# Kernel tuning notes

Measured on AMD Instinct MI355X. Metric: run time of the kernel, lower is better.

## Reference

```python
import jax, jax.numpy as jnp
import numpy as np

# Model dims (see init_kwargs)
NU = 4096   # num_users (one-hot feature dim)
NV = 4096   # num_items
C = 5       # num_classes (rating levels)
H0 = 256    # hidden[0]
H1 = 128    # hidden[1]
D_IN = 512  # input_dim (side-feature dense dim)
SIDE = 1024 # raw side-feature dim (u_features.size(1))
NB = 2      # nb basis matrices in bilinear decoder


def setup_inputs() -> dict:
    key = jax.random.key(0)
    ks = jax.random.split(key, 16)
    u = jax.random.randint(ks[0], (4096,), 0, NU)
    v = jax.random.randint(ks[1], (4096,), 0, NV)
    r = jax.random.randint(ks[2], (4096,), 0, C)  # unused by forward (as in source)
    raw = jax.random.randint(ks[3], (NU, NV), 0, 4 * C)
    adj_matrix = (raw[None, :, :] == jnp.arange(1, C + 1)[:, None, None]).astype(jnp.float32)
    u_features = jax.random.normal(ks[4], (NU, SIDE), jnp.float32)
    v_features = jax.random.normal(ks[5], (NV, SIDE), jnp.float32)
    def w(k, shape, fan):
        return jax.random.normal(k, shape, jnp.float32) / np.float32(np.sqrt(fan))
    u_w = w(ks[6], (C, NU, H0), NU)          # per-relation GraphConvolution user weights
    v_w = w(ks[7], (C, NV, H0), NV)          # per-relation item weights
    Wu1 = w(ks[8], (D_IN, SIDE), SIDE); bu1 = jnp.zeros((D_IN,), jnp.float32)
    Wv1 = w(ks[9], (D_IN, SIDE), SIDE); bv1 = jnp.zeros((D_IN,), jnp.float32)
    Wu2 = w(ks[10], (H1, D_IN + H0), D_IN + H0)
    Wv2 = w(ks[11], (H1, D_IN + H0), D_IN + H0)
    P = w(ks[12], (NB, H1, H1), H1)          # bilinear basis matrices
    a = w(ks[13], (NB, C), NB)               # basis -> class coefficients
    return dict(u=u, v=v, r=r, adj_matrix=adj_matrix, u_features=u_features,
                v_features=v_features, u_w=u_w, v_w=v_w, Wu1=Wu1, bu1=bu1,
                Wv1=Wv1, bv1=bv1, Wu2=Wu2, Wv2=Wv2, P=P, a=a)


def reference(u, v, r, adj_matrix, u_features, v_features, u_w, v_w,
              Wu1, bu1, Wv1, bv1, Wu2, Wv2, P, a):
    # m = adj[:, u][:, :, v]  -> [C, nu, nv]
    m = adj_matrix[:, u][:, :, v]
    # degree normalization exactly as written in gc_encoder
    du = jnp.abs(m.sum(axis=1).sum(axis=0))   # [nv]
    di = jnp.abs(m.sum(axis=2).sum(axis=0))   # [nu]
    c = 1.0 / jnp.concatenate([du, di], axis=0)
    c = jnp.where(jnp.isinf(c), jnp.zeros_like(c), c)
    # ordinal weight sharing: W_r = sum_{s<=r} Theta_s; one-hot feat @ W == gather rows
    cu = jnp.cumsum(u_w, axis=0)              # [C, NU, H0]
    cv = jnp.cumsum(v_w, axis=0)
    u_x = cu[:, u]                            # [C, nu, H0]
    v_x = cv[:, v]                            # [C, nv, H0]
    # accumulate per-relation message passing across all C relations at once
    u_next = jnp.einsum('ruv,rvh->uh', m, v_x)   # [nu, H0]
    v_next = jnp.einsum('ruv,ruh->vh', m, u_x)   # [nv, H0]
    z = jax.nn.relu(jnp.concatenate([u_next, v_next], axis=0) * c[:, None])
    nu = u.shape[0]
    u_z, v_z = z[:nu], z[nu:]
    u_f = jax.nn.relu(u_features[u] @ Wu1.T + bu1)
    v_f = jax.nn.relu(v_features[v] @ Wv1.T + bv1)
    u_h = jax.nn.relu(jnp.concatenate([u_z, u_f], axis=1) @ Wu2.T)   # [nu, H1]
    v_h = jax.nn.relu(jnp.concatenate([v_z, v_f], axis=1) @ Wv2.T)   # [nv, H1]
    # bilinear mixture decoder: logits[c,u,v] = sum_b a[b,c] * u_h Q_b v_h^T
    outputs = jnp.einsum('ud,bde,ve,bc->cuv', u_h, P, v_h, a)        # [C, nu, nv]
    logp = jax.nn.log_softmax(outputs, axis=0)
    prob = jnp.exp(logp)
    ratings = jnp.arange(1, C + 1, dtype=outputs.dtype)
    m_hat = jnp.einsum('c,cuv->uv', ratings, prob)
    # losses over observed entries
    mask = m.sum(axis=0) > 0
    n_obs = jnp.maximum(mask.sum(), 1).astype(outputs.dtype)
    loss = -(m * logp).sum() / n_obs
    target = (jnp.argmax(m, axis=0) + 1).astype(outputs.dtype)
    se = jnp.where(mask, (m_hat - target) ** 2, jnp.zeros_like(m_hat))
    rmse_loss = jnp.sqrt(se.sum() / n_obs)
    return (m_hat, loss, rmse_loss)
```

## Files before the change

### kernel.cpp

```cpp
#include <hip/hip_runtime.h>
#include <stdint.h>

#define N4   4096
#define H0   256
#define SIDE 1024
#define DIN  512
#define HCAT 768
#define H1   128
#define NC   5
#define NUV  16777216ULL
#define CAP  1536

typedef __attribute__((ext_vector_type(8))) short short8;
typedef __attribute__((ext_vector_type(4))) float floatx4;

__device__ __forceinline__ unsigned short f2bf(float f) {
    unsigned int u;
    __builtin_memcpy(&u, &f, 4);
    unsigned int r = (u + 0x7FFFu + ((u >> 16) & 1u)) >> 16;
    return (unsigned short)r;
}

__device__ __forceinline__ float bf2f(unsigned short b) {
    unsigned int u = (unsigned int)b << 16;
    float f;
    __builtin_memcpy(&f, &u, 4);
    return f;
}

__global__ __launch_bounds__(256) void k_codeF(const float* __restrict__ adj,
                                               uchar4* __restrict__ code4,
                                               const int* __restrict__ u,
                                               const int* __restrict__ v,
                                               int* __restrict__ cu,
                                               int* __restrict__ cv) {
    int b = blockIdx.x, t = threadIdx.x;
    if (b < 16384) {
        size_t g = (size_t)b * 256 + t;
        size_t base = g * 4;
        uchar4 out = {0, 0, 0, 0};
        #pragma unroll
        for (int c = 0; c < NC; c++) {
            float4 s = *(const float4*)(adj + (size_t)c * NUV + base);
            out.x = (s.x != 0.f) ? (unsigned char)(c + 1) : out.x;
            out.y = (s.y != 0.f) ? (unsigned char)(c + 1) : out.y;
            out.z = (s.z != 0.f) ? (unsigned char)(c + 1) : out.z;
            out.w = (s.w != 0.f) ? (unsigned char)(c + 1) : out.w;
        }
        code4[g] = out;
    } else {
        int i = (b - 16384) * 256 + t;
        atomicAdd(&cu[u[i]], 1);
        atomicAdd(&cv[v[i]], 1);
    }
}

__global__ __launch_bounds__(256) void k_fuse0(const uint8_t* __restrict__ code,
                                               uint8_t* __restrict__ codeT,
                                               const float* __restrict__ u_w,
                                               const int* __restrict__ cnt_u,
                                               unsigned short* __restrict__ T_Au,
                                               const float* __restrict__ v_w,
                                               const int* __restrict__ cnt_v,
                                               unsigned short* __restrict__ T_Bv) {
    __shared__ __align__(16) uint8_t tile[64][80];
    int b = blockIdx.x, t = threadIdx.x;
    if (b < 4096) {
        int bx = b & 63, by = b >> 6;
        int row = t >> 2;
        int seg = (t & 3) * 16;
        int p0 = by * 64, q0 = bx * 64;
        uint4 vdat = *(const uint4*)(code + (size_t)(p0 + row) * N4 + q0 + seg);
        *(uint4*)(&tile[row][seg]) = vdat;
        __syncthreads();
        union { uint4 u4; uint8_t bb[16]; } o;
        #pragma unroll
        for (int l = 0; l < 16; l++) o.bb[l] = tile[seg + l][row];
        *(uint4*)(codeT + (size_t)(q0 + row) * N4 + p0 + seg) = o.u4;
    } else {
        int node = (b - 4096) & 4095;
        int side = (b - 4096) >> 12;
        const float* w = side ? v_w : u_w;
        const int* cnt = side ? cnt_v : cnt_u;
        unsigned short* out = side ? T_Bv : T_Au;
        int h = t;
        float c = (float)cnt[node];
        float acc = 0.f;
        #pragma unroll
        for (int r = 0; r < NC; r++) {
            size_t idx = ((size_t)r * N4 + node) * H0 + h;
            acc += w[idx];
            union { _Float16 h16; unsigned short s; } cvt;
            cvt.h16 = (_Float16)(acc * c);
            out[idx] = cvt.s;
        }
    }
}

__global__ __launch_bounds__(256) void k_prep(const uint8_t* __restrict__ code,
                                              const uint8_t* __restrict__ codeT,
                                              const int* __restrict__ cnt_u,
                                              const int* __restrict__ cnt_v,
                                              unsigned short* __restrict__ idxU,
                                              int* __restrict__ nnzU,
                                              float* __restrict__ rowDeg,
                                              unsigned short* __restrict__ idxV,
                                              int* __restrict__ nnzV,
                                              float* __restrict__ colDeg,
                                              const float* __restrict__ u_feat,
                                              unsigned short* __restrict__ fuhi,
                                              unsigned short* __restrict__ fulo,
                                              const float* __restrict__ v_feat,
                                              unsigned short* __restrict__ fvhi,
                                              unsigned short* __restrict__ fvlo,
                                              const float* __restrict__ Wu1,
                                              unsigned short* __restrict__ wuhi,
                                              unsigned short* __restrict__ wulo,
                                              const float* __restrict__ Wv1,
                                              unsigned short* __restrict__ wvhi,
                                              unsigned short* __restrict__ wvlo,
                                              const float* __restrict__ Wu2,
                                              unsigned short* __restrict__ w2uhi,
                                              unsigned short* __restrict__ w2ulo,
                                              const float* __restrict__ Wv2,
                                              unsigned short* __restrict__ w2vhi,
                                              unsigned short* __restrict__ w2vlo,
                                              const float* __restrict__ P,
                                              unsigned short* __restrict__ pthi,
                                              unsigned short* __restrict__ ptlo) {
    __shared__ float cw[4096];
    __shared__ int wtot[4];
    __shared__ float wdeg[4];
    __shared__ __align__(16) unsigned short ebuf[CAP];
    int b = blockIdx.x, t = threadIdx.x;
    if (b < 8192) {
        int side = b >> 12;
        int p = b & 4095;
        const uint8_t* codeRows = side ? codeT : code;
        const int* cntOther = side ? cnt_u : cnt_v;
        unsigned short* idx = side ? idxV : idxU;
        int* nnz = side ? nnzV : nnzU;
        float* deg = side ? colDeg : rowDeg;

        int lane = t & 63, wv = t >> 6;
        const int4* co4 = (const int4*)cntOther;
        #pragma unroll
        for (int l = 0; l < 4; l++) {
            int4 ci = co4[t + l * 256];
            ((float4*)cw)[t + l * 256] =
                make_float4((float)ci.x, (float)ci.y, (float)ci.z, (float)ci.w);
        }
        uint4 w = ((const uint4*)(codeRows + (size_t)p * N4))[t];
        unsigned char bb[16];
        __builtin_memcpy(bb, &w, 16);
        int cnt = 0;
        #pragma unroll
        for (int j = 0; j < 16; j++) cnt += (bb[j] != 0);
        int sc = cnt;
        #pragma unroll
        for (int off = 1; off < 64; off <<= 1) {
            int up = __shfl_up(sc, off, 64);
            if (lane >= off) sc += up;
        }
        if (lane == 63) wtot[wv] = sc;
        __syncthreads();
        int wbase = 0;
        #pragma unroll
        for (int ww = 0; ww < 4; ww++) wbase += (ww < wv) ? wtot[ww] : 0;
        int total = wtot[0] + wtot[1] + wtot[2] + wtot[3];
        int pos = wbase + sc - cnt;
        float dsum = 0.f;
        #pragma unroll
        for (int j = 0; j < 16; j++) {
            int r = bb[j];
            if (r) {
                int q = t * 16 + j;
                if (pos < CAP) ebuf[pos] = (unsigned short)((r - 1) * N4 + q);
                pos++;
                dsum += cw[q];
            }
        }
        #pragma unroll
        for (int off = 32; off; off >>= 1) dsum += __shfl_down(dsum, off, 64);
        if (lane == 0) wdeg[wv] = dsum;
        __syncthreads();
        int tw = total < CAP ? total : CAP;
        if (t == 0) { deg[p] = wdeg[0] + wdeg[1] + wdeg[2] + wdeg[3]; nnz[p] = tw; }
        for (int e = t; e < tw; e += 256) idx[(size_t)p * CAP + e] = ebuf[e];
        return;
    }
    if (b >= 17600) {
        int tid = (b - 17600) * 256 + t;
        int bb = tid >> 14;
        int d = (tid >> 7) & 127;
        int e = tid & 127;
        float val = P[tid];
        unsigned short hb = f2bf(val);
        size_t o = ((size_t)bb * 128 + e) * 128 + d;
        pthi[o] = hb;
        ptlo[o] = f2bf(val - bf2f(hb));
        return;
    }
    const float* src;
    unsigned short* hi;
    unsigned short* lo;
    int lb;
    if (b < 12288)      { src = u_feat; hi = fuhi; lo = fulo; lb = b - 8192; }
    else if (b < 16384) { src = v_feat; hi = fvhi; lo = fvlo; lb = b - 12288; }
    else if (b < 16896) { src = Wu1; hi = wuhi; lo = wulo; lb = b - 16384; }
    else if (b < 17408) { src = Wv1; hi = wvhi; lo = wvlo; lb = b - 16896; }
    else if (b < 17504) { src = Wu2; hi = w2uhi; lo = w2ulo; lb = b - 17408; }
    else                { src = Wv2; hi = w2vhi; lo = w2vlo; lb = b - 17504; }
    size_t g = ((size_t)lb * 256 + t) * 4;
    float4 x = *(const float4*)(src + g);
    float f[4] = {x.x, x.y, x.z, x.w};
    unsigned short hh[4], ll[4];
    #pragma unroll
    for (int k = 0; k < 4; k++) {
        unsigned short hb = f2bf(f[k]);
        hh[k] = hb;
        ll[k] = f2bf(f[k] - bf2f(hb));
    }
    *(ushort4*)(hi + g) = make_ushort4(hh[0], hh[1], hh[2], hh[3]);
    *(ushort4*)(lo + g) = make_ushort4(ll[0], ll[1], ll[2], ll[3]);
}

__global__ __launch_bounds__(256) void k_gatherE(const unsigned short* __restrict__ idxU,
                                                 const int* __restrict__ nnzU,
                                                 const unsigned short* __restrict__ T_Bv,
                                                 const unsigned short* __restrict__ idxV,
                                                 const int* __restrict__ nnzV,
                                                 const unsigned short* __restrict__ T_Au,
                                                 float* __restrict__ pnn) {
    __shared__ __align__(16) unsigned short sidx[CAP];
    __shared__ float red[16][132];
    __shared__ int sbnd[2];
    int bid = blockIdx.x;
    int side  = bid >> 15;
    int r1    = bid & 32767;
    int epoch = r1 >> 13;
    int r2    = r1 & 8191;
    int p     = r2 >> 1;
    int half  = r2 & 1;

    const unsigned short* idx = side ? idxV : idxU;
    const int* nnz = side ? nnzV : nnzU;
    const char* tb = (const char*)(side ? T_Au : T_Bv);

    int t = threadIdx.x;
    int n = nnz[p];
    const unsigned short* rowIdx = idx + (size_t)p * CAP;
    int nv = (n + 7) >> 3;
    for (int i = t; i < nv; i += 256)
        ((uint4*)sidx)[i] = ((const uint4*)rowIdx)[i];
    __syncthreads();
    if (t < 2) {
        int target = (epoch + t) << 10;
        int lo = 0, hi = n;
        while (lo < hi) {
            int mid = (lo + hi) >> 1;
            int q = sidx[mid] & 4095;
            if (q < target) lo = mid + 1; else hi = mid;
        }
        sbnd[t] = lo;
    }
    __syncthreads();
    int elo = sbnd[0], ehi = sbnd[1];

    int s = t >> 4;
    int c = t & 15;
    int boff = half * 256 + c * 16;
    float acc[8] = {0.f, 0.f, 0.f, 0.f, 0.f, 0.f, 0.f, 0.f};
    int cnt = ehi - elo;
    int nmain = elo + (cnt & ~63);
    for (int e = elo + s; e < nmain; e += 64) {
        int o0 = ((int)sidx[e])      << 9;
        int o1 = ((int)sidx[e + 16]) << 9;
        int o2 = ((int)sidx[e + 32]) << 9;
        int o3 = ((int)sidx[e + 48]) << 9;
        uint4 d0 = *(const uint4*)(tb + o0 + boff);
        uint4 d1 = *(const uint4*)(tb + o1 + boff);
        uint4 d2 = *(const uint4*)(tb + o2 + boff);
        uint4 d3 = *(const uint4*)(tb + o3 + boff);
        union { uint4 u; _Float16 h[8]; } cv;
        cv.u = d0;
        #pragma unroll
        for (int k = 0; k < 8; k++) acc[k] += (float)cv.h[k];
        cv.u = d1;
        #pragma unroll
        for (int k = 0; k < 8; k++) acc[k] += (float)cv.h[k];
        cv.u = d2;
        #pragma unroll
        for (int k = 0; k < 8; k++) acc[k] += (float)cv.h[k];
        cv.u = d3;
        #pragma unroll
        for (int k = 0; k < 8; k++) acc[k] += (float)cv.h[k];
    }
    for (int e = nmain + s; e < ehi; e += 16) {
        int o = ((int)sidx[e]) << 9;
        uint4 d = *(const uint4*)(tb + o + boff);
        union { uint4 u; _Float16 h[8]; } cv;
        cv.u = d;
        #pragma unroll
        for (int k = 0; k < 8; k++) acc[k] += (float)cv.h[k];
    }
    #pragma unroll
    for (int k = 0; k < 8; k++) red[s][c * 8 + k] = acc[k];
    __syncthreads();
    if (t < 128) {
        float sum = 0.f;
        #pragma unroll
        for (int ss = 0; ss < 16; ss++) sum += red[ss][t];
        pnn[(((size_t)(side * 4 + epoch)) * N4 + p) * H0 + half * 128 + t] = sum;
    }
}

__global__ __launch_bounds__(256) void k_l1Z(const unsigned short* __restrict__ fuhi,
                                             const unsigned short* __restrict__ fulo,
                                             const unsigned short* __restrict__ fvhi,
                                             const unsigned short* __restrict__ fvlo,
                                             const int* __restrict__ u,
                                             const int* __restrict__ v,
                                             const unsigned short* __restrict__ wuhi,
                                             const unsigned short* __restrict__ wulo,
                                             const unsigned short* __restrict__ wvhi,
                                             const unsigned short* __restrict__ wvlo,
                                             const float* __restrict__ bu1,
                                             const float* __restrict__ bv1,
                                             unsigned short* __restrict__ chiU,
                                             unsigned short* __restrict__ cloU,
                                             unsigned short* __restrict__ chiV,
                                             unsigned short* __restrict__ cloV,
                                             const float* __restrict__ pnn,
                                             const float* __restrict__ colDeg,
                                             const float* __restrict__ rowDeg,
                                             const uint8_t* __restrict__ code,
                                             uint8_t* __restrict__ codeR) {
    __shared__ __align__(16) unsigned short Bh[64][72];
    __shared__ __align__(16) unsigned short Bl[64][72];
    int b = blockIdx.x, t = threadIdx.x;
    if (b < 1024) {
        int side = b >> 9;
        int rem = b & 511;
        const unsigned short* Ahi = side ? fvhi : fuhi;
        const unsigned short* Alo = side ? fvlo : fulo;
        const int* rowmap = side ? v : u;
        const unsigned short* Bhi = side ? wvhi : wuhi;
        const unsigned short* Blo = side ? wvlo : wulo;
        const float* bias = side ? bv1 : bu1;
        unsigned short* CHi = (side ? chiV : chiU) + H0;
        unsigned short* CLo = (side ? cloV : cloU) + H0;

        int wave = t >> 6, lane = t & 63;
        int lr = lane & 15;
        int lk = lane >> 4;
        int i0 = (rem >> 3) * 64 + wave * 16;
        int n0 = (rem & 7) * 64;
        int gi = rowmap[i0 + lr];
        const unsigned short* pah = Ahi + (size_t)gi * SIDE;
        const unsigned short* pal = Alo + (size_t)gi * SIDE;
        int srow = t >> 2, sseg = (t & 3) * 16;
        floatx4 acc[4];
        #pragma unroll
        for (int jt = 0; jt < 4; jt++) acc[jt] = (floatx4){0.f, 0.f, 0.f, 0.f};
        for (int ks = 0; ks < SIDE / 64; ks++) {
            const unsigned short* sh = Bhi + (size_t)(n0 + srow) * SIDE + ks * 64 + sseg;
            const unsigned short* sl = Blo + (size_t)(n0 + srow) * SIDE + ks * 64 + sseg;
            __syncthreads();
            *(uint4*)(&Bh[srow][sseg]) = *(const uint4*)sh;
            *(uint4*)(&Bh[srow][sseg + 8]) = *(const uint4*)(sh + 8);
            *(uint4*)(&Bl[srow][sseg]) = *(const uint4*)sl;
            *(uint4*)(&Bl[srow][sseg + 8]) = *(const uint4*)(sl + 8);
            __syncthreads();
            #pragma unroll
            for (int kk = 0; kk < 2; kk++) {
                int ko = ks * 64 + kk * 32 + lk * 8;
                short8 ah = *(const short8*)(pah + ko);
                short8 al = *(const short8*)(pal + ko);
                #pragma unroll
                for (int jt = 0; jt < 4; jt++) {
                    short8 bh = *(const short8*)(&Bh[jt * 16 + lr][kk * 32 + lk * 8]);
                    short8 bl = *(const short8*)(&Bl[jt * 16 + lr][kk * 32 + lk * 8]);
                    acc[jt] = __builtin_amdgcn_mfma_f32_16x16x32_bf16(ah, bh, acc[jt], 0, 0, 0);
                    acc[jt] = __builtin_amdgcn_mfma_f32_16x16x32_bf16(ah, bl, acc[jt], 0, 0, 0);
                    acc[jt] = __builtin_amdgcn_mfma_f32_16x16x32_bf16(al, bh, acc[jt], 0, 0, 0);
                }
            }
        }
        #pragma unroll
        for (int jt = 0; jt < 4; jt++) {
            int cn = n0 + jt * 16 + lr;
            float bb = bias[cn];
            #pragma unroll
            for (int r = 0; r < 4; r++) {
                int ci = i0 + lk * 4 + r;
                float vv = fmaxf(acc[jt][r] + bb, 0.f);
                unsigned short hb = f2bf(vv);
                CHi[(size_t)ci * HCAT + cn] = hb;
                CLo[(size_t)ci * HCAT + cn] = f2bf(vv - bf2f(hb));
            }
        }
        return;
    }
    if (b < 9216) {
        int idx = b - 1024;
        int side = idx >> 12;
        int i = idx & 4095;
        const int* idxs = side ? v : u;
        const int* idxo = side ? u : v;
        const float* deg = side ? rowDeg : colDeg;
        unsigned short* catHi = side ? chiV : chiU;
        unsigned short* catLo = side ? cloV : cloU;
        int h = t;
        float d = deg[idxo[i]];
        float inv = d > 0.f ? 1.f / d : 0.f;
        int row = idxs[i];
        const float* pr = pnn + ((size_t)side * 4 * N4 + row) * H0 + h;
        float nnv = 0.f;
        #pragma unroll
        for (int e = 0; e < 4; e++) nnv += pr[(size_t)e * N4 * H0];
        float val = fmaxf(nnv * inv, 0.f);
        unsigned short hb = f2bf(val);
        catHi[(size_t)i * HCAT + h] = hb;
        catLo[(size_t)i * HCAT + h] = f2bf(val - bf2f(hb));
        return;
    }
    uint8_t* rowbuf = (uint8_t*)Bh;
    int i = b - 9216;
    int urow = u[i];
    ((uint4*)rowbuf)[t] = ((const uint4*)(code + (size_t)urow * N4))[t];
    __syncthreads();
    uint8_t ob[16];
    #pragma unroll
    for (int w = 0; w < 4; w++) {
        int4 vv = ((const int4*)v)[t * 4 + w];
        ob[w * 4 + 0] = rowbuf[vv.x];
        ob[w * 4 + 1] = rowbuf[vv.y];
        ob[w * 4 + 2] = rowbuf[vv.z];
        ob[w * 4 + 3] = rowbuf[vv.w];
    }
    uint4 o;
    __builtin_memcpy(&o, ob, 16);
    ((uint4*)(codeR + (size_t)i * N4))[t] = o;
}

__global__ __launch_bounds__(256) void k_l2F(const unsigned short* __restrict__ chiU,
                                             const unsigned short* __restrict__ cloU,
                                             const unsigned short* __restrict__ w2uhi,
                                             const unsigned short* __restrict__ w2ulo,
                                             unsigned short* __restrict__ uhhi,
                                             unsigned short* __restrict__ uhlo,
                                             const unsigned short* __restrict__ chiV,
                                             const unsigned short* __restrict__ cloV,
                                             const unsigned short* __restrict__ w2vhi,
                                             const unsigned short* __restrict__ w2vlo,
                                             unsigned short* __restrict__ vhb) {
    __shared__ __align__(16) unsigned short Bh[64][72];
    __shared__ __align__(16) unsigned short Bl[64][72];
    int side = blockIdx.z;
    const unsigned short* Ahi = side ? chiV : chiU;
    const unsigned short* Alo = side ? cloV : cloU;
    const unsigned short* Bhi = side ? w2vhi : w2uhi;
    const unsigned short* Blo = side ? w2vlo : w2ulo;

    int t = threadIdx.x;
    int wave = t >> 6, lane = t & 63;
    int lr = lane & 15;
    int lk = lane >> 4;
    int i0 = blockIdx.y * 64 + wave * 16;
    int n0 = blockIdx.x * 64;
    const unsigned short* pah = Ahi + (size_t)(i0 + lr) * HCAT;
    const unsigned short* pal = Alo + (size_t)(i0 + lr) * HCAT;
    int srow = t >> 2, sseg = (t & 3) * 16;
    floatx4 acc[4];
    #pragma unroll
    for (int jt = 0; jt < 4; jt++) acc[jt] = (floatx4){0.f, 0.f, 0.f, 0.f};
    for (int ks = 0; ks < HCAT / 64; ks++) {
        const unsigned short* sh = Bhi + (size_t)(n0 + srow) * HCAT + ks * 64 + sseg;
        const unsigned short* sl = Blo + (size_t)(n0 + srow) * HCAT + ks * 64 + sseg;
        __syncthreads();
        *(uint4*)(&Bh[srow][sseg]) = *(const uint4*)sh;
        *(uint4*)(&Bh[srow][sseg + 8]) = *(const uint4*)(sh + 8);
        *(uint4*)(&Bl[srow][sseg]) = *(const uint4*)sl;
        *(uint4*)(&Bl[srow][sseg + 8]) = *(const uint4*)(sl + 8);
        __syncthreads();
        #pragma unroll
        for (int kk = 0; kk < 2; kk++) {
            int ko = ks * 64 + kk * 32 + lk * 8;
            short8 ah = *(const short8*)(pah + ko);
            short8 al = *(const short8*)(pal + ko);
            #pragma unroll
            for (int jt = 0; jt < 4; jt++) {
                short8 bh = *(const short8*)(&Bh[jt * 16 + lr][kk * 32 + lk * 8]);
                short8 bl = *(const short8*)(&Bl[jt * 16 + lr][kk * 32 + lk * 8]);
                acc[jt] = __builtin_amdgcn_mfma_f32_16x16x32_bf16(ah, bh, acc[jt], 0, 0, 0);
                acc[jt] = __builtin_amdgcn_mfma_f32_16x16x32_bf16(ah, bl, acc[jt], 0, 0, 0);
                acc[jt] = __builtin_amdgcn_mfma_f32_16x16x32_bf16(al, bh, acc[jt], 0, 0, 0);
            }
        }
    }
    #pragma unroll
    for (int jt = 0; jt < 4; jt++) {
        int cn = n0 + jt * 16 + lr;
        #pragma unroll
        for (int r = 0; r < 4; r++) {
            int ci = i0 + lk * 4 + r;
            float vv = fmaxf(acc[jt][r], 0.f);
            if (side) {
                vhb[(size_t)ci * H1 + cn] = f2bf(vv);
            } else {
                unsigned short hb = f2bf(vv);
                uhhi[(size_t)ci * H1 + cn] = hb;
                uhlo[(size_t)ci * H1 + cn] = f2bf(vv - bf2f(hb));
            }
        }
    }
}

__global__ __launch_bounds__(256) void k_tb(const unsigned short* __restrict__ uhhi,
                                            const unsigned short* __restrict__ uhlo,
                                            const unsigned short* __restrict__ pthi,
                                            const unsigned short* __restrict__ ptlo,
                                            unsigned short* __restrict__ tbout) {
    __shared__ __align__(16) unsigned short Bh[64][72];
    __shared__ __align__(16) unsigned short Bl[64][72];
    int bmat = blockIdx.z;
    int t = threadIdx.x;
    int wave = t >> 6, lane = t & 63;
    int lr = lane & 15;
    int lk = lane >> 4;
    int i0 = blockIdx.y * 64 + wave * 16;
    int n0 = blockIdx.x * 64;
    const unsigned short* Bhi = pthi + (size_t)bmat * H1 * H1;
    const unsigned short* Blo = ptlo + (size_t)bmat * H1 * H1;
    const unsigned short* pah = uhhi + (size_t)(i0 + lr) * H1;
    const unsigned short* pal = uhlo + (size_t)(i0 + lr) * H1;
    int srow = t >> 2, sseg = (t & 3) * 16;
    floatx4 acc[4];
    #pragma unroll
    for (int jt = 0; jt < 4; jt++) acc[jt] = (floatx4){0.f, 0.f, 0.f, 0.f};
    for (int ks = 0; ks < H1 / 64; ks++) {
        const unsigned short* sh = Bhi + (size_t)(n0 + srow) * H1 + ks * 64 + sseg;
        const unsigned short* sl = Blo + (size_t)(n0 + srow) * H1 + ks * 64 + sseg;
        __syncthreads();
        *(uint4*)(&Bh[srow][sseg]) = *(const uint4*)sh;
        *(uint4*)(&Bh[srow][sseg + 8]) = *(const uint4*)(sh + 8);
        *(uint4*)(&Bl[srow][sseg]) = *(const uint4*)sl;
        *(uint4*)(&Bl[srow][sseg + 8]) = *(const uint4*)(sl + 8);
        __syncthreads();
        #pragma unroll
        for (int kk = 0; kk < 2; kk++) {
            int ko = ks * 64 + kk * 32 + lk * 8;
            short8 ah = *(const short8*)(pah + ko);
            short8 al = *(const short8*)(pal + ko);
            #pragma unroll
            for (int jt = 0; jt < 4; jt++) {
                short8 bh = *(const short8*)(&Bh[jt * 16 + lr][kk * 32 + lk * 8]);
                short8 bl = *(const short8*)(&Bl[jt * 16 + lr][kk * 32 + lk * 8]);
                acc[jt] = __builtin_amdgcn_mfma_f32_16x16x32_bf16(ah, bh, acc[jt], 0, 0, 0);
                acc[jt] = __builtin_amdgcn_mfma_f32_16x16x32_bf16(ah, bl, acc[jt], 0, 0, 0);
                acc[jt] = __builtin_amdgcn_mfma_f32_16x16x32_bf16(al, bh, acc[jt], 0, 0, 0);
            }
        }
    }
    #pragma unroll
    for (int jt = 0; jt < 4; jt++) {
        int cn = n0 + jt * 16 + lr;
        #pragma unroll
        for (int r = 0; r < 4; r++) {
            int ci = i0 + lk * 4 + r;
            tbout[(size_t)bmat * N4 * H1 + (size_t)ci * H1 + cn] = f2bf(acc[jt][r]);
        }
    }
}

__global__ __launch_bounds__(256) void k_scores3(const unsigned short* __restrict__ tb,
                                                 const unsigned short* __restrict__ vhb,
                                                 const uint8_t* __restrict__ codeR,
                                                 const float* __restrict__ a_f,
                                                 float* __restrict__ mhat,
                                                 float* __restrict__ part) {
    __shared__ float wred[4][3];
    int t = threadIdx.x;
    int wave = t >> 6, lane = t & 63;
    int lr = lane & 15;
    int lk = lane >> 4;
    int i0 = blockIdx.y * 64 + wave * 16;
    int j0 = blockIdx.x * 128;
    float sa0[NC], sa1[NC];
    #pragma unroll
    for (int c = 0; c < NC; c++) { sa0[c] = a_f[c]; sa1[c] = a_f[5 + c]; }

    const unsigned short* t0p = tb;
    const unsigned short* t1p = tb + (size_t)N4 * H1;
    short8 a0[4], a1[4];
    #pragma unroll
    for (int kc = 0; kc < 4; kc++) {
        size_t off = (size_t)(i0 + lr) * H1 + kc * 32 + lk * 8;
        a0[kc] = *(const short8*)(t0p + off);
        a1[kc] = *(const short8*)(t1p + off);
    }

    const uint8_t* crbase = codeR + (size_t)(i0 + lk * 4) * N4 + lr;
    short8 bcur[4];
    int cbv[4];
    {
        int jb = j0;
        const uint8_t* crp = crbase + jb;
        cbv[0] = crp[0];
        cbv[1] = crp[N4];
        cbv[2] = crp[2 * N4];
        cbv[3] = crp[3 * N4];
        #pragma unroll
        for (int kc = 0; kc < 4; kc++)
            bcur[kc] = *(const short8*)(vhb + (size_t)(jb + lr) * H1 + kc * 32 + lk * 8);
    }

    float lsum = 0.f, ssum = 0.f, nobs = 0.f;
    for (int jt = 0; jt < 8; jt++) {
        int jb = j0 + jt * 16;
        int j = jb + lr;
        short8 bnext[4];
        int cbn[4];
        if (jt < 7) {
            int jb2 = jb + 16;
            const uint8_t* crp = crbase + jb2;
            cbn[0] = crp[0];
            cbn[1] = crp[N4];
            cbn[2] = crp[2 * N4];
            cbn[3] = crp[3 * N4];
            #pragma unroll
            for (int kc = 0; kc < 4; kc++)
                bnext[kc] = *(const short8*)(vhb + (size_t)(jb2 + lr) * H1 + kc * 32 + lk * 8);
        }
        floatx4 C0 = {0.f, 0.f, 0.f, 0.f}, C1 = {0.f, 0.f, 0.f, 0.f};
        #pragma unroll
        for (int kc = 0; kc < 4; kc++) {
            C0 = __builtin_amdgcn_mfma_f32_16x16x32_bf16(a0[kc], bcur[kc], C0, 0, 0, 0);
            C1 = __builtin_amdgcn_mfma_f32_16x16x32_bf16(a1[kc], bcur[kc], C1, 0, 0, 0);
        }
        #pragma unroll
        for (int r = 0; r < 4; r++) {
            int i = i0 + lk * 4 + r;
            float v0 = C0[r], v1 = C1[r];
            float l[NC];
            float mx = -1e30f;
            #pragma unroll
            for (int c = 0; c < NC; c++) {
                l[c] = sa0[c] * v0 + sa1[c] * v1;
                mx = fmaxf(mx, l[c]);
            }
            float den = 0.f, num = 0.f;
            #pragma unroll
            for (int c = 0; c < NC; c++) {
                float e = __expf(l[c] - mx);
                den += e;
                num += (float)(c + 1) * e;
            }
            float mh = num / den;
            mhat[(size_t)i * N4 + j] = mh;
            int cb = cbv[r];
            if (cb) {
                float lse = mx + __logf(den);
                lsum += lse - l[cb - 1];
                float df = mh - (float)cb;
                ssum += df * df;
                nobs += 1.f;
            }
        }
        if (jt < 7) {
            #pragma unroll
            for (int kc = 0; kc < 4; kc++) bcur[kc] = bnext[kc];
            #pragma unroll
            for (int r = 0; r < 4; r++) cbv[r] = cbn[r];
        }
    }
    #pragma unroll
    for (int off = 32; off; off >>= 1) {
        lsum += __shfl_down(lsum, off, 64);
        ssum += __shfl_down(ssum, off, 64);
        nobs += __shfl_down(nobs, off, 64);
    }
    if (lane == 0) { wred[wave][0] = lsum; wred[wave][1] = ssum; wred[wave][2] = nobs; }
    __syncthreads();
    if (t == 0) {
        int bid = blockIdx.y * gridDim.x + blockIdx.x;
        part[bid * 3 + 0] = wred[0][0] + wred[1][0] + wred[2][0] + wred[3][0];
        part[bid * 3 + 1] = wred[0][1] + wred[1][1] + wred[2][1] + wred[3][1];
        part[bid * 3 + 2] = wred[0][2] + wred[1][2] + wred[2][2] + wred[3][2];
    }
}

__global__ __launch_bounds__(256) void k_finalize(const float* __restrict__ part,
                                                  float* __restrict__ out) {
    __shared__ float sred[3][4];
    int t = threadIdx.x, lane = t & 63, wv = t >> 6;
    float l = 0.f, s = 0.f, n = 0.f;
    for (int i = t; i < 2048; i += 256) {
        l += part[i * 3 + 0];
        s += part[i * 3 + 1];
        n += part[i * 3 + 2];
    }
    #pragma unroll
    for (int off = 32; off; off >>= 1) {
        l += __shfl_down(l, off, 64);
        s += __shfl_down(s, off, 64);
        n += __shfl_down(n, off, 64);
    }
    if (lane == 0) { sred[0][wv] = l; sred[1][wv] = s; sred[2][wv] = n; }
    __syncthreads();
    if (t == 0) {
        float L = sred[0][0] + sred[0][1] + sred[0][2] + sred[0][3];
        float S = sred[1][0] + sred[1][1] + sred[1][2] + sred[1][3];
        float N = fmaxf(sred[2][0] + sred[2][1] + sred[2][2] + sred[2][3], 1.f);
        out[NUV + 0] = L / N;
        out[NUV + 1] = sqrtf(S / N);
    }
}

extern "C" void kernel_launch(void* const* d_in, const int* in_sizes, int n_in,
                              void* d_out, int out_size, void* d_ws, size_t ws_size,
                              hipStream_t stream) {
    const int* u = (const int*)d_in[0];
    const int* v = (const int*)d_in[1];
    const float* adj    = (const float*)d_in[3];
    const float* u_feat = (const float*)d_in[4];
    const float* v_feat = (const float*)d_in[5];
    const float* u_w    = (const float*)d_in[6];
    const float* v_w    = (const float*)d_in[7];
    const float* Wu1    = (const float*)d_in[8];
    const float* bu1    = (const float*)d_in[9];
    const float* Wv1    = (const float*)d_in[10];
    const float* bv1    = (const float*)d_in[11];
    const float* Wu2    = (const float*)d_in[12];
    const float* Wv2    = (const float*)d_in[13];
    const float* P      = (const float*)d_in[14];
    const float* a      = (const float*)d_in[15];
    float* out = (float*)d_out;

    char* ws = (char*)d_ws;
    const size_t O_CODE  = 0;
    const size_t O_CNTU  = 16777216;
    const size_t O_CNTV  = O_CNTU + 16384;
    const size_t O_ACC   = O_CNTV + 16384;
    const size_t O_TAU   = O_ACC + 256;
    const size_t O_TBV   = O_TAU + 10485760;
    const size_t O_IDXU  = O_TBV + 10485760;
    const size_t O_IDXV  = O_IDXU + 12582912;
    const size_t O_NNZU  = O_IDXV + 12582912;
    const size_t O_NNZV  = O_NNZU + 16384;
    const size_t O_RDEG  = O_NNZV + 16384;
    const size_t O_CDEG  = O_RDEG + 16384;
    const size_t O_UNN   = O_CDEG + 16384;
    const size_t O_VNN   = O_UNN + 4194304;
    const size_t O_UCAT  = O_VNN + 4194304;
    const size_t O_VCAT  = O_UCAT + 12582912;
    const size_t O_UH    = O_VCAT + 12582912;
    const size_t O_VHB   = O_UH + 2097152;
    const size_t O_PT    = O_VHB + 1048576;
    const size_t O_TB    = O_PT + 131072;
    const size_t O_CODET = O_UCAT;
    const size_t O_CODER = O_TAU;
    const size_t O_PART  = O_CNTU;
    const size_t O_FULO  = O_UNN;
    const size_t O_CHIU  = O_UCAT;
    const size_t O_CLOU  = O_UCAT + 6291456;
    const size_t O_CHIV  = O_VCAT;
    const size_t O_CLOV  = O_VCAT + 6291456;
    const size_t S_FVHI  = 0;
    const size_t S_FVLO  = 8388608;
    const size_t S_WUHI  = 16777216;
    const size_t S_WULO  = S_WUHI + 1048576;
    const size_t S_WVHI  = S_WULO + 1048576;
    const size_t S_WVLO  = S_WVHI + 1048576;
    const size_t S_W2UHI = S_WVLO + 1048576;
    const size_t S_W2ULO = S_W2UHI + 196608;
    const size_t S_W2VHI = S_W2ULO + 196608;
    const size_t S_W2VLO = S_W2VHI + 196608;
    const size_t S_PNN   = 25165824;
    const size_t S_FUHI  = 58720256;

    uint8_t* code  = (uint8_t*)(ws + O_CODE);
    uint8_t* codeT = (uint8_t*)(ws + O_CODET);
    uint8_t* codeR = (uint8_t*)(ws + O_CODER);
    int* cnt_u = (int*)(ws + O_CNTU);
    int* cnt_v = (int*)(ws + O_CNTV);
    unsigned short* T_Au = (unsigned short*)(ws + O_TAU);
    unsigned short* T_Bv = (unsigned short*)(ws + O_TBV);
    unsigned short* idxU = (unsigned short*)(ws + O_IDXU);
    unsigned short* idxV = (unsigned short*)(ws + O_IDXV);
    int* nnzU = (int*)(ws + O_NNZU);
    int* nnzV = (int*)(ws + O_NNZV);
    float* rowDeg = (float*)(ws + O_RDEG);
    float* colDeg = (float*)(ws + O_CDEG);
    unsigned short* uhhi = (unsigned short*)(ws + O_UH);
    unsigned short* uhlo = (unsigned short*)(ws + O_UH + 1048576);
    unsigned short* vhb = (unsigned short*)(ws + O_VHB);
    unsigned short* pthi = (unsigned short*)(ws + O_PT);
    unsigned short* ptlo = (unsigned short*)(ws + O_PT + 65536);
    unsigned short* tb = (unsigned short*)(ws + O_TB);
    float* part = (float*)(ws + O_PART);
    unsigned short* fulo = (unsigned short*)(ws + O_FULO);
    unsigned short* chiU = (unsigned short*)(ws + O_CHIU);
    unsigned short* cloU = (unsigned short*)(ws + O_CLOU);
    unsigned short* chiV = (unsigned short*)(ws + O_CHIV);
    unsigned short* cloV = (unsigned short*)(ws + O_CLOV);
    char* outc = (char*)d_out;
    unsigned short* fuhi = (unsigned short*)(outc + S_FUHI);
    unsigned short* fvhi = (unsigned short*)(outc + S_FVHI);
    unsigned short* fvlo = (unsigned short*)(outc + S_FVLO);
    unsigned short* wuhi = (unsigned short*)(outc + S_WUHI);
    unsigned short* wulo = (unsigned short*)(outc + S_WULO);
    unsigned short* wvhi = (unsigned short*)(outc + S_WVHI);
    unsigned short* wvlo = (unsigned short*)(outc + S_WVLO);
    unsigned short* w2uhi = (unsigned short*)(outc + S_W2UHI);
    unsigned short* w2ulo = (unsigned short*)(outc + S_W2ULO);
    unsigned short* w2vhi = (unsigned short*)(outc + S_W2VHI);
    unsigned short* w2vlo = (unsigned short*)(outc + S_W2VLO);
    float* pnn = (float*)(outc + S_PNN);

    hipMemsetAsync(ws + O_CNTU, 0, 16384 + 16384, stream);

    k_codeF<<<16400, 256, 0, stream>>>(adj, (uchar4*)code, u, v, cnt_u, cnt_v);
    k_fuse0<<<12288, 256, 0, stream>>>(code, codeT, u_w, cnt_u, T_Au, v_w, cnt_v, T_Bv);
    k_prep<<<17728, 256, 0, stream>>>(code, codeT, cnt_u, cnt_v,
                                      idxU, nnzU, rowDeg, idxV, nnzV, colDeg,
                                      u_feat, fuhi, fulo,
                                      v_feat, fvhi, fvlo,
                                      Wu1, wuhi, wulo, Wv1, wvhi, wvlo,
                                      Wu2, w2uhi, w2ulo, Wv2, w2vhi, w2vlo,
                                      P, pthi, ptlo);
    k_gatherE<<<65536, 256, 0, stream>>>(idxU, nnzU, T_Bv, idxV, nnzV, T_Au, pnn);
    k_l1Z<<<13312, 256, 0, stream>>>(fuhi, fulo, fvhi, fvlo, u, v,
                                     wuhi, wulo, wvhi, wvlo, bu1, bv1,
                                     chiU, cloU, chiV, cloV,
                                     pnn, colDeg, rowDeg, code, codeR);
    k_l2F<<<dim3(2, 64, 2), 256, 0, stream>>>(chiU, cloU, w2uhi, w2ulo, uhhi, uhlo,
                                              chiV, cloV, w2vhi, w2vlo, vhb);
    k_tb<<<dim3(2, 64, 2), 256, 0, stream>>>(uhhi, uhlo, pthi, ptlo, tb);
    k_scores3<<<dim3(32, 64), 256, 0, stream>>>(tb, vhb, codeR, a, out, part);
    k_finalize<<<1, 256, 0, stream>>>(part, out);
}
```

Before: 874.0 us.

## Merge layer-1 GEMM into gather kernel and fold finalize into scores via last-block atomic

The dense layer-1 side-feature GEMM blocks, which do not depend on the gather results, now share a launch with the sparse gather blocks so both run in one grid. The z-normalisation and codeR rows move into a separate k_zR kernel. The single-block finalize kernel is removed: the last k_scores3 block, found with an atomic counter, does the final reduction. This cuts launch gaps and lets the independent GEMM overlap with the gather, but the shared-memory union and atomic counter add a little complexity.

```diff
diff --git a/kernel.cpp b/kernel.cpp
--- a/kernel.cpp
+++ b/kernel.cpp
@@ -225,121 +225,35 @@
     *(ushort4*)(lo + g) = make_ushort4(ll[0], ll[1], ll[2], ll[3]);
 }
 
-__global__ __launch_bounds__(256) void k_gatherE(const unsigned short* __restrict__ idxU,
-                                                 const int* __restrict__ nnzU,
-                                                 const unsigned short* __restrict__ T_Bv,
-                                                 const unsigned short* __restrict__ idxV,
-                                                 const int* __restrict__ nnzV,
-                                                 const unsigned short* __restrict__ T_Au,
-                                                 float* __restrict__ pnn) {
-    __shared__ __align__(16) unsigned short sidx[CAP];
-    __shared__ float red[16][132];
-    __shared__ int sbnd[2];
-    int bid = blockIdx.x;
-    int side  = bid >> 15;
-    int r1    = bid & 32767;
-    int epoch = r1 >> 13;
-    int r2    = r1 & 8191;
-    int p     = r2 >> 1;
-    int half  = r2 & 1;
-
-    const unsigned short* idx = side ? idxV : idxU;
-    const int* nnz = side ? nnzV : nnzU;
-    const char* tb = (const char*)(side ? T_Au : T_Bv);
-
-    int t = threadIdx.x;
-    int n = nnz[p];
-    const unsigned short* rowIdx = idx + (size_t)p * CAP;
-    int nv = (n + 7) >> 3;
-    for (int i = t; i < nv; i += 256)
-        ((uint4*)sidx)[i] = ((const uint4*)rowIdx)[i];
-    __syncthreads();
-    if (t < 2) {
-        int target = (epoch + t) << 10;
-        int lo = 0, hi = n;
-        while (lo < hi) {
-            int mid = (lo + hi) >> 1;
-            int q = sidx[mid] & 4095;
-            if (q < target) lo = mid + 1; else hi = mid;
-        }
-        sbnd[t] = lo;
-    }
-    __syncthreads();
-    int elo = sbnd[0], ehi = sbnd[1];
-
-    int s = t >> 4;
-    int c = t & 15;
-    int boff = half * 256 + c * 16;
-    float acc[8] = {0.f, 0.f, 0.f, 0.f, 0.f, 0.f, 0.f, 0.f};
-    int cnt = ehi - elo;
-    int nmain = elo + (cnt & ~63);
-    for (int e = elo + s; e < nmain; e += 64) {
-        int o0 = ((int)sidx[e])      << 9;
-        int o1 = ((int)sidx[e + 16]) << 9;
-        int o2 = ((int)sidx[e + 32]) << 9;
-        int o3 = ((int)sidx[e + 48]) << 9;
-        uint4 d0 = *(const uint4*)(tb + o0 + boff);
-        uint4 d1 = *(const uint4*)(tb + o1 + boff);
-        uint4 d2 = *(const uint4*)(tb + o2 + boff);
-        uint4 d3 = *(const uint4*)(tb + o3 + boff);
-        union { uint4 u; _Float16 h[8]; } cv;
-        cv.u = d0;
-        #pragma unroll
-        for (int k = 0; k < 8; k++) acc[k] += (float)cv.h[k];
-        cv.u = d1;
-        #pragma unroll
-        for (int k = 0; k < 8; k++) acc[k] += (float)cv.h[k];
-        cv.u = d2;
-        #pragma unroll
-        for (int k = 0; k < 8; k++) acc[k] += (float)cv.h[k];
-        cv.u = d3;
-        #pragma unroll
-        for (int k = 0; k < 8; k++) acc[k] += (float)cv.h[k];
-    }
-    for (int e = nmain + s; e < ehi; e += 16) {
-        int o = ((int)sidx[e]) << 9;
-        uint4 d = *(const uint4*)(tb + o + boff);
-        union { uint4 u; _Float16 h[8]; } cv;
-        cv.u = d;
-        #pragma unroll
-        for (int k = 0; k < 8; k++) acc[k] += (float)cv.h[k];
-    }
-    #pragma unroll
-    for (int k = 0; k < 8; k++) red[s][c * 8 + k] = acc[k];
-    __syncthreads();
-    if (t < 128) {
-        float sum = 0.f;
-        #pragma unroll
-        for (int ss = 0; ss < 16; ss++) sum += red[ss][t];
-        pnn[(((size_t)(side * 4 + epoch)) * N4 + p) * H0 + half * 128 + t] = sum;
-    }
-}
-
-__global__ __launch_bounds__(256) void k_l1Z(const unsigned short* __restrict__ fuhi,
-                                             const unsigned short* __restrict__ fulo,
-                                             const unsigned short* __restrict__ fvhi,
-                                             const unsigned short* __restrict__ fvlo,
-                                             const int* __restrict__ u,
-                                             const int* __restrict__ v,
-                                             const unsigned short* __restrict__ wuhi,
-                                             const unsigned short* __restrict__ wulo,
-                                             const unsigned short* __restrict__ wvhi,
-                                             const unsigned short* __restrict__ wvlo,
-                                             const float* __restrict__ bu1,
-                                             const float* __restrict__ bv1,
-                                             unsigned short* __restrict__ chiU,
-                                             unsigned short* __restrict__ cloU,
-                                             unsigned short* __restrict__ chiV,
-                                             unsigned short* __restrict__ cloV,
-                                             const float* __restrict__ pnn,
-                                             const float* __restrict__ colDeg,
-                                             const float* __restrict__ rowDeg,
-                                             const uint8_t* __restrict__ code,
-                                             uint8_t* __restrict__ codeR) {
-    __shared__ __align__(16) unsigned short Bh[64][72];
-    __shared__ __align__(16) unsigned short Bl[64][72];
+__global__ __launch_bounds__(256) void k_gatherL1(const unsigned short* __restrict__ idxU,
+                                                  const int* __restrict__ nnzU,
+                                                  const unsigned short* __restrict__ T_Bv,
+                                                  const unsigned short* __restrict__ idxV,
+                                                  const int* __restrict__ nnzV,
+                                                  const unsigned short* __restrict__ T_Au,
+                                                  float* __restrict__ pnn,
+                                                  const unsigned short* __restrict__ fuhi,
+                                                  const unsigned short* __restrict__ fulo,
+                                                  const unsigned short* __restrict__ fvhi,
+                                                  const unsigned short* __restrict__ fvlo,
+                                                  const int* __restrict__ u,
+                                                  const int* __restrict__ v,
+                                                  const unsigned short* __restrict__ wuhi,
+                                                  const unsigned short* __restrict__ wulo,
+                                                  const unsigned short* __restrict__ wvhi,
+                                                  const unsigned short* __restrict__ wvlo,
+                                                  const float* __restrict__ bu1,
+                                                  const float* __restrict__ bv1,
+                                                  unsigned short* __restrict__ chiU,
+                                                  unsigned short* __restrict__ cloU,
+                                                  unsigned short* __restrict__ chiV,
+                                                  unsigned short* __restrict__ cloV) {
+    __shared__ __align__(16) char smem[18432];
     int b = blockIdx.x, t = threadIdx.x;
     if (b < 1024) {
+        typedef unsigned short Row72[72];
+        Row72* Bh = (Row72*)smem;
+        Row72* Bl = (Row72*)(smem + 9216);
         int side = b >> 9;
         int rem = b & 511;
         const unsigned short* Ahi = side ? fvhi : fuhi;
@@ -402,10 +316,104 @@
         }
         return;
     }
-    if (b < 9216) {
-        int idx = b - 1024;
-        int side = idx >> 12;
-        int i = idx & 4095;
+    unsigned short* sidx = (unsigned short*)smem;
+    float (*red)[132] = (float(*)[132])(smem + 3072);
+    int* sbnd = (int*)(smem + 3072 + 8448);
+    int bid = b - 1024;
+    int side  = bid >> 15;
+    int r1    = bid & 32767;
+    int epoch = r1 >> 13;
+    int r2    = r1 & 8191;
+    int p     = r2 >> 1;
+    int half  = r2 & 1;
+
+    const unsigned short* idx = side ? idxV : idxU;
+    const int* nnz = side ? nnzV : nnzU;
+    const char* tb = (const char*)(side ? T_Au : T_Bv);
+
+    int n = nnz[p];
+    const unsigned short* rowIdx = idx + (size_t)p * CAP;
+    int nv = (n + 7) >> 3;
+    for (int i = t; i < nv; i += 256)
+        ((uint4*)sidx)[i] = ((const uint4*)rowIdx)[i];
+    __syncthreads();
+    if (t < 2) {
+        int target = (epoch + t) << 10;
+        int lo = 0, hi = n;
+        while (lo < hi) {
+            int mid = (lo + hi) >> 1;
+            int q = sidx[mid] & 4095;
+            if (q < target) lo = mid + 1; else hi = mid;
+        }
+        sbnd[t] = lo;
+    }
+    __syncthreads();
+    int elo = sbnd[0], ehi = sbnd[1];
+
+    int s = t >> 4;
+    int c = t & 15;
+    int boff = half * 256 + c * 16;
+    float acc[8] = {0.f, 0.f, 0.f, 0.f, 0.f, 0.f, 0.f, 0.f};
+    int cnt = ehi - elo;
+    int nmain = elo + (cnt & ~63);
+    for (int e = elo + s; e < nmain; e += 64) {
+        int o0 = ((int)sidx[e])      << 9;
+        int o1 = ((int)sidx[e + 16]) << 9;
+        int o2 = ((int)sidx[e + 32]) << 9;
+        int o3 = ((int)sidx[e + 48]) << 9;
+        uint4 d0 = *(const uint4*)(tb + o0 + boff);
+        uint4 d1 = *(const uint4*)(tb + o1 + boff);
+        uint4 d2 = *(const uint4*)(tb + o2 + boff);
+        uint4 d3 = *(const uint4*)(tb + o3 + boff);
+        union { uint4 u; _Float16 h[8]; } cv;
+        cv.u = d0;
+        #pragma unroll
+        for (int k = 0; k < 8; k++) acc[k] += (float)cv.h[k];
+        cv.u = d1;
+        #pragma unroll
+        for (int k = 0; k < 8; k++) acc[k] += (float)cv.h[k];
+        cv.u = d2;
+        #pragma unroll
+        for (int k = 0; k < 8; k++) acc[k] += (float)cv.h[k];
+        cv.u = d3;
+        #pragma unroll
+        for (int k = 0; k < 8; k++) acc[k] += (float)cv.h[k];
+    }
+    for (int e = nmain + s; e < ehi; e += 16) {
+        int o = ((int)sidx[e]) << 9;
+        uint4 d = *(const uint4*)(tb + o + boff);
+        union { uint4 u; _Float16 h[8]; } cv;
+        cv.u = d;
+        #pragma unroll
+        for (int k = 0; k < 8; k++) acc[k] += (float)cv.h[k];
+    }
+    #pragma unroll
+    for (int k = 0; k < 8; k++) red[s][c * 8 + k] = acc[k];
+    __syncthreads();
+    if (t < 128) {
+        float sum = 0.f;
+        #pragma unroll
+        for (int ss = 0; ss < 16; ss++) sum += red[ss][t];
+        pnn[(((size_t)(side * 4 + epoch)) * N4 + p) * H0 + half * 128 + t] = sum;
+    }
+}
+
+__global__ __launch_bounds__(256) void k_zR(const int* __restrict__ u,
+                                            const int* __restrict__ v,
+                                            const float* __restrict__ pnn,
+                                            const float* __restrict__ colDeg,
+                                            const float* __restrict__ rowDeg,
+                                            unsigned short* __restrict__ chiU,
+                                            unsigned short* __restrict__ cloU,
+                                            unsigned short* __restrict__ chiV,
+                                            unsigned short* __restrict__ cloV,
+                                            const uint8_t* __restrict__ code,
+                                            uint8_t* __restrict__ codeR) {
+    __shared__ __align__(16) uint8_t rowbuf[4096];
+    int b = blockIdx.x, t = threadIdx.x;
+    if (b < 8192) {
+        int side = b >> 12;
+        int i = b & 4095;
         const int* idxs = side ? v : u;
         const int* idxo = side ? u : v;
         const float* deg = side ? rowDeg : colDeg;
@@ -425,8 +433,7 @@
         catLo[(size_t)i * HCAT + h] = f2bf(val - bf2f(hb));
         return;
     }
-    uint8_t* rowbuf = (uint8_t*)Bh;
-    int i = b - 9216;
+    int i = b - 8192;
     int urow = u[i];
     ((uint4*)rowbuf)[t] = ((const uint4*)(code + (size_t)urow * N4))[t];
     __syncthreads();
@@ -579,8 +586,11 @@
                                                  const uint8_t* __restrict__ codeR,
                                                  const float* __restrict__ a_f,
                                                  float* __restrict__ mhat,
-                                                 float* __restrict__ part) {
+                                                 float* __restrict__ part,
+                                                 unsigned int* __restrict__ dcnt) {
     __shared__ float wred[4][3];
+    __shared__ float sred[3][4];
+    __shared__ bool islast;
     int t = threadIdx.x;
     int wave = t >> 6, lane = t & 63;
     int lr = lane & 15;
@@ -688,13 +698,13 @@
         part[bid * 3 + 0] = wred[0][0] + wred[1][0] + wred[2][0] + wred[3][0];
         part[bid * 3 + 1] = wred[0][1] + wred[1][1] + wred[2][1] + wred[3][1];
         part[bid * 3 + 2] = wred[0][2] + wred[1][2] + wred[2][2] + wred[3][2];
-    }
-}
-
-__global__ __launch_bounds__(256) void k_finalize(const float* __restrict__ part,
-                                                  float* __restrict__ out) {
-    __shared__ float sred[3][4];
-    int t = threadIdx.x, lane = t & 63, wv = t >> 6;
+        __threadfence();
+        unsigned int done = atomicAdd(dcnt, 1u);
+        islast = (done == 2047u);
+    }
+    __syncthreads();
+    if (!islast) return;
+    __threadfence();
     float l = 0.f, s = 0.f, n = 0.f;
     for (int i = t; i < 2048; i += 256) {
         l += part[i * 3 + 0];
@@ -707,14 +717,14 @@
         s += __shfl_down(s, off, 64);
         n += __shfl_down(n, off, 64);
     }
-    if (lane == 0) { sred[0][wv] = l; sred[1][wv] = s; sred[2][wv] = n; }
+    if (lane == 0) { sred[0][wave] = l; sred[1][wave] = s; sred[2][wave] = n; }
     __syncthreads();
     if (t == 0) {
         float L = sred[0][0] + sred[0][1] + sred[0][2] + sred[0][3];
         float S = sred[1][0] + sred[1][1] + sred[1][2] + sred[1][3];
         float N = fmaxf(sred[2][0] + sred[2][1] + sred[2][2] + sred[2][3], 1.f);
-        out[NUV + 0] = L / N;
-        out[NUV + 1] = sqrtf(S / N);
+        mhat[NUV + 0] = L / N;
+        mhat[NUV + 1] = sqrtf(S / N);
     }
 }
 
@@ -785,6 +795,7 @@
     uint8_t* codeR = (uint8_t*)(ws + O_CODER);
     int* cnt_u = (int*)(ws + O_CNTU);
     int* cnt_v = (int*)(ws + O_CNTV);
+    unsigned int* dcnt = (unsigned int*)(ws + O_ACC);
     unsigned short* T_Au = (unsigned short*)(ws + O_TAU);
     unsigned short* T_Bv = (unsigned short*)(ws + O_TBV);
     unsigned short* idxU = (unsigned short*)(ws + O_IDXU);
@@ -819,7 +830,7 @@
     unsigned short* w2vlo = (unsigned short*)(outc + S_W2VLO);
     float* pnn = (float*)(outc + S_PNN);
 
-    hipMemsetAsync(ws + O_CNTU, 0, 16384 + 16384, stream);
+    hipMemsetAsync(ws + O_CNTU, 0, 16384 + 16384 + 256, stream);
 
     k_codeF<<<16400, 256, 0, stream>>>(adj, (uchar4*)code, u, v, cnt_u, cnt_v);
     k_fuse0<<<12288, 256, 0, stream>>>(code, codeT, u_w, cnt_u, T_Au, v_w, cnt_v, T_Bv);
@@ -830,14 +841,14 @@
                                       Wu1, wuhi, wulo, Wv1, wvhi, wvlo,
                                       Wu2, w2uhi, w2ulo, Wv2, w2vhi, w2vlo,
                                       P, pthi, ptlo);
-    k_gatherE<<<65536, 256, 0, stream>>>(idxU, nnzU, T_Bv, idxV, nnzV, T_Au, pnn);
-    k_l1Z<<<13312, 256, 0, stream>>>(fuhi, fulo, fvhi, fvlo, u, v,
-                                     wuhi, wulo, wvhi, wvlo, bu1, bv1,
-                                     chiU, cloU, chiV, cloV,
-                                     pnn, colDeg, rowDeg, code, codeR);
+    k_gatherL1<<<66560, 256, 0, stream>>>(idxU, nnzU, T_Bv, idxV, nnzV, T_Au, pnn,
+                                          fuhi, fulo, fvhi, fvlo, u, v,
+                                          wuhi, wulo, wvhi, wvlo, bu1, bv1,
+                                          chiU, cloU, chiV, cloV);
+    k_zR<<<12288, 256, 0, stream>>>(u, v, pnn, colDeg, rowDeg,
+                                    chiU, cloU, chiV, cloV, code, codeR);
     k_l2F<<<dim3(2, 64, 2), 256, 0, stream>>>(chiU, cloU, w2uhi, w2ulo, uhhi, uhlo,
                                               chiV, cloV, w2vhi, w2vlo, vhb);
     k_tb<<<dim3(2, 64, 2), 256, 0, stream>>>(uhhi, uhlo, pthi, ptlo, tb);
-    k_scores3<<<dim3(32, 64), 256, 0, stream>>>(tb, vhb, codeR, a, out, part);
-    k_finalize<<<1, 256, 0, stream>>>(part, out);
-}
+    k_scores3<<<dim3(32, 64), 256, 0, stream>>>(tb, vhb, codeR, a, out, part, dcnt);
+}
```

Result: slower. 1.018 ms (+16.4%).
